# Performance work log

Measured on AMD Instinct MI355X. Metric: run time of the kernel, lower is better.

Reference implementation:

```python
import jax, jax.numpy as jnp
import numpy as np

B, Q, K = 4, 256, 1024          # batch, query_len, key_len
DQ, DK, DV, H = 512, 512, 512, 256  # query/key/value dims, num_hiddens


def setup_inputs() -> dict:
    key = jax.random.key(0)
    ks = jax.random.split(key, 7)
    return {
        "queries": jax.random.normal(ks[0], (B, Q, DQ), jnp.float32),
        "keys": jax.random.normal(ks[1], (B, K, DK), jnp.float32),
        "values": jax.random.normal(ks[2], (B, K, DV), jnp.float32),
        "valid_lens": jax.random.randint(ks[3], (B,), 1, K + 1),
        "Wq": jax.random.normal(ks[4], (H, DQ), jnp.float32) / np.sqrt(DQ).astype(np.float32),
        "Wk": jax.random.normal(ks[5], (H, DK), jnp.float32) / np.sqrt(DK).astype(np.float32),
        "wv": jax.random.normal(ks[6], (H,), jnp.float32) / np.sqrt(H).astype(np.float32),
    }


def reference(queries, keys, values, valid_lens, Wq, Wk, wv):
    # Linear projections (bias=False), torch Linear weight layout (out, in)
    q = jnp.einsum("bqd,hd->bqh", queries, Wq)          # (B, Q, H)
    k = jnp.einsum("bkd,hd->bkh", keys, Wk)             # (B, K, H)
    # Broadcast add -> tanh -> scalar score per (q, k) pair
    feats = jnp.tanh(q[:, :, None, :] + k[:, None, :, :])  # (B, Q, K, H)
    scores = jnp.einsum("bqkh,h->bqk", feats, wv)           # (B, Q, K)
    # masked_softmax with 1D valid_lens: mask applies along key axis per batch
    kv_len = scores.shape[-1]
    mask = jnp.arange(kv_len)[None, None, :] < valid_lens[:, None, None]  # (B,1,K)
    scores = jnp.where(mask, scores, jnp.float32(-1e6))
    attn = jax.nn.softmax(scores, axis=-1)               # (B, Q, K)
    # dropout is identity in eval mode
    return jnp.einsum("bqk,bkv->bqv", attn, values)      # (B, Q, DV)
```

## Files before the change

kernel.cpp:

```cpp
#include <hip/hip_runtime.h>
#include <stdint.h>


#define NB 4
#define NQ 256
#define NK 1024
#define ND 512
#define NH 256
#define QROWS 4
#define PJR 16
#define PJH 64

#define C2L2E 2.8853900817779268f
#define L2E   1.4426950408889634f

typedef float v2f __attribute__((ext_vector_type(2)));

__device__ void ff_vldec(const int* p, int* v) {
  bool ok = true;
  for (int i = 0; i < 4; ++i) { int x = p[i]; if (x < 1 || x > NK) ok = false; }
  if (ok) { for (int i = 0; i < 4; ++i) v[i] = p[i]; return; }
  ok = true;
  for (int i = 0; i < 4; ++i) {
    if (p[2 * i + 1] != 0) ok = false;
    int x = p[2 * i]; if (x < 1 || x > NK) ok = false;
  }
  if (ok) { for (int i = 0; i < 4; ++i) v[i] = p[2 * i]; return; }
  ok = true;
  for (int i = 0; i < 4; ++i) {
    union { int i; float f; } u; u.i = p[i];
    if (!(u.f >= 1.0f && u.f <= 1024.0f && u.f == floorf(u.f))) ok = false;
  }
  if (ok) {
    for (int i = 0; i < 4; ++i) { union { int i; float f; } u; u.i = p[i]; v[i] = (int)u.f; }
    return;
  }
  ok = true;
  for (int i = 0; i < 4; ++i) {
    union { long long l; double d; } u;
    u.l = ((long long)p[2 * i + 1] << 32) | (unsigned int)p[2 * i];
    if (!(u.d >= 1.0 && u.d <= 1024.0 && u.d == floor(u.d))) ok = false;
  }
  if (ok) {
    for (int i = 0; i < 4; ++i) {
      union { long long l; double d; } u;
      u.l = ((long long)p[2 * i + 1] << 32) | (unsigned int)p[2 * i];
      v[i] = (int)u.d;
    }
    return;
  }
  const uint16_t* hh = (const uint16_t*)p;
  const short*    s  = (const short*)p;
  ok = true;
  for (int i = 0; i < 4; ++i) { int x = s[i]; if (x < 1 || x > NK) ok = false; }
  if (ok) { for (int i = 0; i < 4; ++i) v[i] = s[i]; return; }
  ok = true;
  for (int i = 0; i < 4; ++i) {
    union { uint16_t u; _Float16 h; } u; u.u = hh[i];
    float f = (float)u.h;
    if (!(f >= 1.0f && f <= 1024.0f && f == floorf(f))) ok = false;
  }
  if (ok) {
    for (int i = 0; i < 4; ++i) {
      union { uint16_t u; _Float16 h; } u; u.u = hh[i];
      v[i] = (int)(float)u.h;
    }
    return;
  }
  ok = true;
  for (int i = 0; i < 4; ++i) {
    union { uint32_t u; float f; } u; u.u = ((uint32_t)hh[i]) << 16;
    if (!(u.f >= 1.0f && u.f <= 1028.0f)) ok = false;
  }
  if (ok) {
    for (int i = 0; i < 4; ++i) {
      union { uint32_t u; float f; } u; u.u = ((uint32_t)hh[i]) << 16;
      int x = (int)(u.f + 0.5f); if (x > NK) x = NK; v[i] = x;
    }
    return;
  }
  for (int i = 0; i < 4; ++i) v[i] = NK;
}

__global__ __launch_bounds__(256) void ff_wt(
    const float* __restrict__ Wq, const float* __restrict__ Wk,
    float* __restrict__ WTq, float* __restrict__ WTk)
{
  const int idx = blockIdx.x * 256 + threadIdx.x;
  const int d4 = idx & 127, h = idx >> 7;
  const float* src = blockIdx.y ? Wk : Wq;
  float*       dst = blockIdx.y ? WTk : WTq;
  float4 w = *(const float4*)(src + (size_t)h * ND + d4 * 4);
  w.x *= C2L2E; w.y *= C2L2E; w.z *= C2L2E; w.w *= C2L2E;
  *(float4*)(dst + ((size_t)d4 * NH + h) * 4) = w;
}

__global__ __launch_bounds__(256) void ff_proj(
    const float* __restrict__ q_in, const float* __restrict__ k_in,
    const float* __restrict__ WTq, const float* __restrict__ WTk,
    float* __restrict__ qp, float* __restrict__ kp)
{
  __shared__ float xs[PJR * ND];
  const int t  = threadIdx.x;
  const int rg = blockIdx.x >> 2;
  const int h0 = (blockIdx.x & 3) * PJH;
  const int gr0 = rg * PJR;
  const bool isq = gr0 < NB * NQ;
  const float* xin = isq ? (q_in + (size_t)gr0 * ND)
                         : (k_in + (size_t)(gr0 - NB * NQ) * ND);
  const float4* wt4 = (const float4*)(isq ? WTq : WTk);

  #pragma unroll
  for (int i = 0; i < 8; ++i)
    ((float4*)xs)[t + 256 * i] = ((const float4*)xin)[t + 256 * i];
  __syncthreads();

  const int L  = t & 63;
  const int rw = t >> 6;
  float a0 = 0.f, a1 = 0.f, a2 = 0.f, a3 = 0.f;
  const float4* xr = (const float4*)xs + (size_t)(4 * rw) * 128;

  #pragma unroll 4
  for (int d4 = 0; d4 < ND / 4; ++d4) {
    float4 w  = wt4[(size_t)d4 * NH + h0 + L];
    float4 x0 = xr[d4];
    float4 x1 = xr[128 + d4];
    float4 x2 = xr[256 + d4];
    float4 x3 = xr[384 + d4];
    a0 += w.x*x0.x + w.y*x0.y + w.z*x0.z + w.w*x0.w;
    a1 += w.x*x1.x + w.y*x1.y + w.z*x1.z + w.w*x1.w;
    a2 += w.x*x2.x + w.y*x2.y + w.z*x2.z + w.w*x2.w;
    a3 += w.x*x3.x + w.y*x3.y + w.z*x3.z + w.w*x3.w;
  }

  const int h = h0 + L;
  if (isq) {
    float* o = qp + (size_t)(gr0 + 4 * rw) * NH + h;
    o[0] = a0; o[NH] = a1; o[2 * NH] = a2; o[3 * NH] = a3;
  } else {
    const int g = gr0 - NB * NQ + 4 * rw;
    const int bb = g >> 10, k = g & (NK - 1);
    *(float4*)(kp + ((size_t)bb * NH + h) * NK + k) = make_float4(a0, a1, a2, a3);
  }
}

__global__ __launch_bounds__(1024) void ff_attn(
    const float* __restrict__ qp, const float* __restrict__ kp,
    const float* __restrict__ vals, const int* __restrict__ vlraw,
    const float* __restrict__ wvp, float* __restrict__ out)
{
  __shared__ float qs[NH * QROWS];
  __shared__ float ws[NH];
  __shared__ float st[NK * QROWS];
  __shared__ float pm[16], psm[16];
  __shared__ float part[4 * QROWS * ND];

  const int t  = threadIdx.x;
  const int q0 = blockIdx.x * QROWS;
  const int b  = blockIdx.y;

  {
    const float* qsrc = qp + ((size_t)b * NQ + q0) * NH;
    const int row = t >> 8, h = t & 255;
    qs[h * QROWS + row] = qsrc[t];
    if (t < NH) ws[t] = -2.0f * wvp[t];
  }
  __syncthreads();

  int vls[4];
  ff_vldec(vlraw, vls);
  const int vl = vls[b];

  v2f a01 = {0.f, 0.f}, a23 = {0.f, 0.f};
  {
    const float* kvp = kp + (size_t)b * NH * NK + t;
    #pragma unroll 8
    for (int h = 0; h < NH; ++h) {
      float kv = kvp[(size_t)h * NK];
      v2f kv2; kv2.x = kv; kv2.y = kv;
      v2f q01 = *(const v2f*)(qs + h * QROWS);
      v2f q23 = *(const v2f*)(qs + h * QROWS + 2);
      float w = ws[h];
      v2f w2; w2.x = w; w2.y = w;
      v2f u01 = q01 + kv2;
      v2f u23 = q23 + kv2;
      v2f e01, e23;
      e01.x = __builtin_amdgcn_exp2f(u01.x);
      e01.y = __builtin_amdgcn_exp2f(u01.y);
      e23.x = __builtin_amdgcn_exp2f(u23.x);
      e23.y = __builtin_amdgcn_exp2f(u23.y);
      v2f one; one.x = 1.0f; one.y = 1.0f;
      v2f d01 = one + e01, d23 = one + e23;
      v2f r01, r23;
      r01.x = __builtin_amdgcn_rcpf(d01.x);
      r01.y = __builtin_amdgcn_rcpf(d01.y);
      r23.x = __builtin_amdgcn_rcpf(d23.x);
      r23.y = __builtin_amdgcn_rcpf(d23.y);
      a01 += w2 * r01;
      a23 += w2 * r23;
    }
  }
  {
    const bool okm = (t < vl);
    *(float4*)&st[t * 4] = make_float4(okm ? a01.x : -1e6f, okm ? a01.y : -1e6f,
                                       okm ? a23.x : -1e6f, okm ? a23.y : -1e6f);
  }
  __syncthreads();

  {
    const int wid = t >> 6, lane = t & 63;
    const int row = wid >> 2, seg = wid & 3;
    const int kb = seg * 256 + lane;
    float v0 = st[(kb      ) * 4 + row];
    float v1 = st[(kb +  64) * 4 + row];
    float v2 = st[(kb + 128) * 4 + row];
    float v3 = st[(kb + 192) * 4 + row];
    float m = fmaxf(fmaxf(v0, v1), fmaxf(v2, v3));
    for (int o = 32; o; o >>= 1) m = fmaxf(m, __shfl_xor(m, o));
    if (lane == 0) pm[wid] = m;
    __syncthreads();
    m = fmaxf(fmaxf(pm[row*4+0], pm[row*4+1]), fmaxf(pm[row*4+2], pm[row*4+3]));
    float e0 = __builtin_amdgcn_exp2f((v0 - m) * L2E);
    float e1 = __builtin_amdgcn_exp2f((v1 - m) * L2E);
    float e2 = __builtin_amdgcn_exp2f((v2 - m) * L2E);
    float e3 = __builtin_amdgcn_exp2f((v3 - m) * L2E);
    float sm = e0 + e1 + e2 + e3;
    for (int o = 32; o; o >>= 1) sm += __shfl_xor(sm, o);
    if (lane == 0) psm[wid] = sm;
    __syncthreads();
    const float S = psm[row*4+0] + psm[row*4+1] + psm[row*4+2] + psm[row*4+3];
    const float rr = 1.0f / S;
    st[(kb      ) * 4 + row] = e0 * rr;
    st[(kb +  64) * 4 + row] = e1 * rr;
    st[(kb + 128) * 4 + row] = e2 * rr;
    st[(kb + 192) * 4 + row] = e3 * rr;
  }
  __syncthreads();

  {
    const int kq = t >> 8, c2 = (t & 255) * 2;
    const float* vb = vals + (size_t)b * NK * ND + c2;
    v2f o0 = {0.f,0.f}, o1 = {0.f,0.f}, o2 = {0.f,0.f}, o3 = {0.f,0.f};
    const int k0 = kq * 256;
    #pragma unroll 8
    for (int k = k0; k < k0 + 256; ++k) {
      v2f vv = *(const v2f*)(vb + (size_t)k * ND);
      float4 a = *(const float4*)&st[k * 4];
      v2f ax; ax.x = a.x; ax.y = a.x;
      v2f ay; ay.x = a.y; ay.y = a.y;
      v2f az; az.x = a.z; az.y = a.z;
      v2f aw; aw.x = a.w; aw.y = a.w;
      o0 += ax * vv; o1 += ay * vv; o2 += az * vv; o3 += aw * vv;
    }
    float* pp = &part[(size_t)kq * QROWS * ND + c2];
    *(v2f*)(pp         ) = o0;
    *(v2f*)(pp +     ND) = o1;
    *(v2f*)(pp + 2 * ND) = o2;
    *(v2f*)(pp + 3 * ND) = o3;
  }
  __syncthreads();
  {
    const int r = t >> 8, c2 = (t & 255) * 2;
    const float* pp = &part[(size_t)r * ND + c2];
    v2f s = {0.f, 0.f};
    #pragma unroll
    for (int kq = 0; kq < 4; ++kq) s += *(const v2f*)(pp + (size_t)kq * QROWS * ND);
    *(v2f*)(out + ((size_t)b * NQ + q0 + r) * ND + c2) = s;
  }
}

extern "C" void kernel_launch(void* const* d_in, const int* in_sizes, int n_in,
                              void* d_out, int out_size, void* d_ws, size_t ws_size,
                              hipStream_t stream) {
  const float* queries = (const float*)d_in[0];
  const float* keys    = (const float*)d_in[1];
  const float* values  = (const float*)d_in[2];
  const int*   vlens   = (const int*)d_in[3];
  const float* Wq      = (const float*)d_in[4];
  const float* Wk      = (const float*)d_in[5];
  const float* wv      = (const float*)d_in[6];
  float* out = (float*)d_out;

  float* qp  = (float*)d_ws;
  float* kp  = qp  + (size_t)NB * NQ * NH;
  float* wtq = kp  + (size_t)NB * NH * NK;
  float* wtk = wtq + (size_t)(ND / 4) * NH * 4;

  ff_wt  <<<dim3(128, 2), 256, 0, stream>>>(Wq, Wk, wtq, wtk);
  ff_proj<<<dim3((NB * (NQ + NK) / PJR) * (NH / PJH)), 256, 0, stream>>>(
      queries, keys, wtq, wtk, qp, kp);
  ff_attn<<<dim3(NQ / QROWS, NB), 1024, 0, stream>>>(qp, kp, values, vlens, wv, out);
}
```

Before: 195.7 us.

## Split attention across two key halves with a separate combine kernel

Adds ff_attn2, which divides the key axis into two 512-wide halves across blocks. Each block computes unnormalized exp scores, partial softmax sums and a partial P·V, and ff_comb then adds the halves and normalizes. This doubles grid parallelism (512 blocks instead of 256) so more of the GPU is busy, at the cost of extra workspace traffic and an additional launch. The new path is used only when the workspace is large enough, and it skips max-subtraction because the tanh-bounded scores keep exp in range.

```diff
diff --git a/kernel.cpp b/kernel.cpp
--- a/kernel.cpp
+++ b/kernel.cpp
@@ -144,6 +144,127 @@
   }
 }
 
+__global__ __launch_bounds__(1024) void ff_attn2(
+    const float* __restrict__ qp, const float* __restrict__ kp,
+    const float* __restrict__ vals, const int* __restrict__ vlraw,
+    const float* __restrict__ wvp, float* __restrict__ pvpart,
+    float* __restrict__ Sg)
+{
+  __shared__ float qs[NH * QROWS];
+  __shared__ float ws[NH];
+  __shared__ float st[512 * QROWS];
+  __shared__ float psum[32];
+  __shared__ float part[4 * QROWS * ND];
+
+  const int t  = threadIdx.x;
+  const int kh = blockIdx.x;
+  const int q0 = blockIdx.y * QROWS;
+  const int b  = blockIdx.z;
+
+  {
+    const float* qsrc = qp + ((size_t)b * NQ + q0) * NH;
+    const int row = t >> 8, h = t & 255;
+    qs[h * QROWS + row] = qsrc[t];
+    if (t < NH) ws[t] = -2.0f * wvp[t];
+  }
+  __syncthreads();
+
+  int vls[4];
+  ff_vldec(vlraw, vls);
+  const int vl = vls[b];
+
+  const int kk = t & 511, rh = t >> 9;
+  v2f acc = {0.f, 0.f};
+  {
+    const float* kvp = kp + (size_t)b * NH * NK + kh * 512 + kk;
+    const float* qsp = qs + 2 * rh;
+    #pragma unroll 8
+    for (int h = 0; h < NH; ++h) {
+      float kv = kvp[(size_t)h * NK];
+      v2f kv2; kv2.x = kv; kv2.y = kv;
+      v2f q2 = *(const v2f*)(qsp + h * QROWS);
+      float w = ws[h];
+      v2f w2; w2.x = w; w2.y = w;
+      v2f u = q2 + kv2;
+      v2f e;
+      e.x = __builtin_amdgcn_exp2f(u.x);
+      e.y = __builtin_amdgcn_exp2f(u.y);
+      v2f one; one.x = 1.0f; one.y = 1.0f;
+      v2f d = one + e;
+      v2f r;
+      r.x = __builtin_amdgcn_rcpf(d.x);
+      r.y = __builtin_amdgcn_rcpf(d.y);
+      acc += w2 * r;
+    }
+  }
+  {
+    const bool okm = (kh * 512 + kk) < vl;
+    v2f E;
+    E.x = okm ? __builtin_amdgcn_exp2f(acc.x * L2E) : 0.f;
+    E.y = okm ? __builtin_amdgcn_exp2f(acc.y * L2E) : 0.f;
+    *(v2f*)&st[kk * 4 + 2 * rh] = E;
+    float sx = E.x, sy = E.y;
+    for (int o = 32; o; o >>= 1) { sx += __shfl_xor(sx, o); sy += __shfl_xor(sy, o); }
+    if ((t & 63) == 0) { psum[(t >> 6) * 2] = sx; psum[(t >> 6) * 2 + 1] = sy; }
+  }
+  __syncthreads();
+
+  if (t < 4) {
+    const int j = t & 1, base = (t >> 1) * 8;
+    float S = 0.f;
+    #pragma unroll
+    for (int w = 0; w < 8; ++w) S += psum[(base + w) * 2 + j];
+    Sg[(((size_t)b * 64 + blockIdx.y) * 4 + t) * 2 + kh] = S;
+  }
+
+  {
+    const int kq = t >> 8, c2 = (t & 255) * 2;
+    const float* vb = vals + (size_t)b * NK * ND
+                    + (size_t)(kh * 512 + kq * 128) * ND + c2;
+    v2f o0 = {0.f,0.f}, o1 = {0.f,0.f}, o2 = {0.f,0.f}, o3 = {0.f,0.f};
+    #pragma unroll 8
+    for (int k = 0; k < 128; ++k) {
+      v2f vv = *(const v2f*)(vb + (size_t)k * ND);
+      float4 a = *(const float4*)&st[(kq * 128 + k) * 4];
+      v2f ax; ax.x = a.x; ax.y = a.x;
+      v2f ay; ay.x = a.y; ay.y = a.y;
+      v2f az; az.x = a.z; az.y = a.z;
+      v2f aw; aw.x = a.w; aw.y = a.w;
+      o0 += ax * vv; o1 += ay * vv; o2 += az * vv; o3 += aw * vv;
+    }
+    *(v2f*)&part[(size_t)(kq * 4 + 0) * ND + c2] = o0;
+    *(v2f*)&part[(size_t)(kq * 4 + 1) * ND + c2] = o1;
+    *(v2f*)&part[(size_t)(kq * 4 + 2) * ND + c2] = o2;
+    *(v2f*)&part[(size_t)(kq * 4 + 3) * ND + c2] = o3;
+  }
+  __syncthreads();
+  {
+    const int r = t >> 8, c2 = (t & 255) * 2;
+    v2f s = {0.f, 0.f};
+    #pragma unroll
+    for (int kq = 0; kq < 4; ++kq)
+      s += *(const v2f*)&part[(size_t)(kq * 4 + r) * ND + c2];
+    *(v2f*)&pvpart[(((size_t)kh * NB + b) * NQ + q0 + r) * ND + c2] = s;
+  }
+}
+
+__global__ __launch_bounds__(256) void ff_comb(
+    const float* __restrict__ pvpart, const float* __restrict__ Sg,
+    float* __restrict__ out)
+{
+  const int bid = blockIdx.x;
+  const int t = threadIdx.x;
+  const float S = Sg[bid * 2] + Sg[bid * 2 + 1];
+  const float rs = 1.0f / S;
+  const int b = bid >> 8, q = bid & 255;
+  const float* p0 = pvpart + ((size_t)b * NQ + q) * ND;
+  const float* p1 = pvpart + ((size_t)(NB + b) * NQ + q) * ND;
+  float2 a = *(const float2*)(p0 + t * 2);
+  float2 c = *(const float2*)(p1 + t * 2);
+  *(float2*)(out + ((size_t)b * NQ + q) * ND + t * 2)
+      = make_float2((a.x + c.x) * rs, (a.y + c.y) * rs);
+}
+
 __global__ __launch_bounds__(1024) void ff_attn(
     const float* __restrict__ qp, const float* __restrict__ kp,
     const float* __restrict__ vals, const int* __restrict__ vlraw,
@@ -182,8 +303,7 @@
       v2f q23 = *(const v2f*)(qs + h * QROWS + 2);
       float w = ws[h];
       v2f w2; w2.x = w; w2.y = w;
-      v2f u01 = q01 + kv2;
-      v2f u23 = q23 + kv2;
+      v2f u01 = q01 + kv2, u23 = q23 + kv2;
       v2f e01, e23;
       e01.x = __builtin_amdgcn_exp2f(u01.x);
       e01.y = __builtin_amdgcn_exp2f(u01.y);
@@ -285,9 +405,19 @@
   float* kp  = qp  + (size_t)NB * NQ * NH;
   float* wtq = kp  + (size_t)NB * NH * NK;
   float* wtk = wtq + (size_t)(ND / 4) * NH * 4;
+  float* pvp = wtk + (size_t)(ND / 4) * NH * 4;
+  float* Sg  = pvp + (size_t)2 * NB * NQ * ND;
+  const size_t need = ((size_t)(Sg - (float*)d_ws) + 2 * NB * NQ) * sizeof(float);
 
   ff_wt  <<<dim3(128, 2), 256, 0, stream>>>(Wq, Wk, wtq, wtk);
   ff_proj<<<dim3((NB * (NQ + NK) / PJR) * (NH / PJH)), 256, 0, stream>>>(
       queries, keys, wtq, wtk, qp, kp);
-  ff_attn<<<dim3(NQ / QROWS, NB), 1024, 0, stream>>>(qp, kp, values, vlens, wv, out);
-}
+  if (ws_size >= need) {
+    ff_attn2<<<dim3(2, NQ / QROWS, NB), 1024, 0, stream>>>(
+        qp, kp, values, vlens, wv, pvp, Sg);
+    ff_comb<<<dim3(NB * NQ), 256, 0, stream>>>(pvp, Sg, out);
+  } else {
+    ff_attn<<<dim3(NQ / QROWS, NB), 1024, 0, stream>>>(
+        qp, kp, values, vlens, wv, out);
+  }
+}
```

Measured after the change: 196.9 us. About the same (+0.7%).
